# Kernel optimization log

Hardware: AMD Instinct MI355X
Metric: run time of the kernel (lower is better)

Reference implementation:

```python
import jax, jax.numpy as jnp
import numpy as np

NUM_GENO = 16384
NUM_ENV = 53
R = 2666
B = 256
EPS = 1e-5


def setup_inputs() -> dict:
    key = jax.random.key(0)
    ks = jax.random.split(key, 12)

    def w(k, shape, fan_in):
        return jax.random.normal(k, shape, dtype=jnp.float32) / np.float32(np.sqrt(fan_in))

    f32 = jnp.float32
    return {
        "x": jax.random.normal(ks[0], (B, NUM_GENO + NUM_ENV), dtype=f32),
        "W1": w(ks[1], (R, NUM_GENO), NUM_GENO), "b1": jnp.zeros((R,), f32),
        "Wmid": w(ks[2], (11, R, R), R), "bmid": jnp.zeros((11, R), f32),
        "bn_g": jnp.ones((12, R), f32), "bn_b": jnp.zeros((12, R), f32),
        "bn_rm": jnp.zeros((12, R), f32), "bn_rv": jnp.ones((12, R), f32),
        "Wlin": w(ks[3], (R, 54, NUM_ENV + 1), NUM_ENV + 1), "blin": jnp.zeros((R, 54), f32),
        "W13": w(ks[4], (54, 54), 54), "b13": jnp.zeros((54,), f32),
        "W14": w(ks[5], (54, 54), 54), "b14": jnp.zeros((54,), f32),
        "W15": w(ks[6], (5, 54), 54), "b15": jnp.zeros((5,), f32),
        "bn3_g": jnp.ones((3, R), f32), "bn3_b": jnp.zeros((3, R), f32),
        "bn3_rm": jnp.zeros((3, R), f32), "bn3_rv": jnp.ones((3, R), f32),
        "W16": w(ks[7], (750, R * 5), R * 5), "b16": jnp.zeros((750,), f32),
        "W17": w(ks[8], (750, 750), 750), "b17": jnp.zeros((750,), f32),
        "W18": w(ks[9], (750, 750), 750), "b18": jnp.zeros((750,), f32),
    }


def reference(x, W1, b1, Wmid, bmid, bn_g, bn_b, bn_rm, bn_rv, Wlin, blin,
              W13, b13, W14, b14, W15, b15, bn3_g, bn3_b, bn3_rm, bn3_rv,
              W16, b16, W17, b17, W18, b18):
    relu = jax.nn.relu

    def bn(h, i):  # BatchNorm1d eval over [B, R]
        return (h - bn_rm[i]) * jax.lax.rsqrt(bn_rv[i] + EPS) * bn_g[i] + bn_b[i]

    env = x[:, NUM_GENO:]           # [B, NUM_ENV]
    h = x[:, :NUM_GENO]             # [B, NUM_GENO]

    h = relu(bn(h @ W1.T + b1, 0))  # fc1; dropout = identity (eval)
    d = h
    k = 0
    for _block in range(5):         # residual blocks: (fc2,fc3) ... (fc10,fc11)
        for _ in range(2):
            h = relu(bn(h @ Wmid[k].T + bmid[k], k + 1))
            k += 1
        h = d + h
        d = h
    h = relu(bn(h @ Wmid[10].T + bmid[10], 11))  # fc12

    # 2666 per-feature tiny Linears fused into one batched GEMM
    # z[b,i,:] = concat(env[b], h[b,i])  -> [B, R, NUM_ENV+1]
    z = jnp.concatenate(
        [jnp.broadcast_to(env[:, None, :], (B, R, NUM_ENV)), h[:, :, None]], axis=-1)
    d3 = jnp.einsum('bif,iof->bio', z, Wlin) + blin[None]  # [B, R, 54]

    def bn3(h3, j):  # BatchNorm1d eval over [B, R, C]: channels = dim 1 (R)
        return ((h3 - bn3_rm[j][None, :, None])
                * jax.lax.rsqrt(bn3_rv[j][None, :, None] + EPS)
                * bn3_g[j][None, :, None] + bn3_b[j][None, :, None])

    h3 = relu(bn3(d3 @ W13.T + b13, 0))
    h3 = relu(bn3(h3 @ W14.T + b14, 1))
    h3 = relu(bn3(h3 @ W15.T + b15, 2))   # [B, R, 5]

    h = h3.reshape(B, -1)                  # [B, R*5]
    h = relu(h @ W16.T + b16)
    h = relu(h @ W17.T + b17)
    h = relu(h @ W18.T + b18)
    return h
```

## Files before the change

### kernel.cpp

```cpp
#include <hip/hip_runtime.h>

#define EPS 1e-5f

typedef __attribute__((ext_vector_type(8))) short s8v;
typedef __attribute__((ext_vector_type(4))) float f4v;

__device__ __forceinline__ unsigned short f2b(float x) {
  unsigned int u = __float_as_uint(x);
  u += 0x7FFFu + ((u >> 16) & 1u);
  return (unsigned short)(u >> 16);
}
__device__ __forceinline__ float b2f(unsigned short b) {
  return __uint_as_float(((unsigned int)b) << 16);
}

__global__ __launch_bounds__(256)
void gemm_bk64(const unsigned short* __restrict__ A, int lda,
               const float* __restrict__ B, int ldb,
               unsigned short* __restrict__ Pb,
               int NPAIR, int N, int K, int kchunk, int KS)
{
  __shared__ unsigned short As[256 * 72];
  __shared__ unsigned short Bs[64 * 72];
  const int bid = (int)blockIdx.x;
  const int ky = bid % KS, ntp = bid / KS;
  const int n0 = ntp << 6;
  const int t = threadIdx.x, lane = t & 63, w = t >> 6;
  const int lr = lane & 15, lk = lane >> 4;

  const int kstart = ky * kchunk;
  const int kend = min(K, kstart + kchunk);
  const int len = kend - kstart;
  const int nfull = len >> 6;
  const int rem = len & 63;

  const int ar = t >> 2, ac = t & 3;
  const int br = t >> 2, bq = t & 3;

  f4v acc[4][4] = {};
  float4 b_cur[4], b_nxt[4];

  auto loadB = [&](float4* dst, int kb) {
    const int row = n0 + br;
    if (row < N) {
      #pragma unroll
      for (int i = 0; i < 4; ++i)
        dst[i] = *(const float4*)(B + (size_t)row * ldb + kb + bq * 16 + i * 4);
    } else {
      #pragma unroll
      for (int i = 0; i < 4; ++i) { dst[i].x = dst[i].y = dst[i].z = dst[i].w = 0.f; }
    }
  };
  auto stageA = [&](int kb) {
    #pragma unroll
    for (int p = 0; p < 4; ++p) {
      const int row = ar + p * 64;
      const s8v v0 = *(const s8v*)(A + (size_t)row * lda + kb + ac * 16);
      const s8v v1 = *(const s8v*)(A + (size_t)row * lda + kb + ac * 16 + 8);
      *(s8v*)(As + row * 72 + ac * 16) = v0;
      *(s8v*)(As + row * 72 + ac * 16 + 8) = v1;
    }
  };
  auto stageB = [&](const float4* bv) {
    s8v p0, p1;
    #pragma unroll
    for (int i = 0; i < 4; ++i) {
      p0[i]     = (short)f2b(bv[i >> 1].x);
    }
    p0[0] = (short)f2b(bv[0].x); p0[1] = (short)f2b(bv[0].y);
    p0[2] = (short)f2b(bv[0].z); p0[3] = (short)f2b(bv[0].w);
    p0[4] = (short)f2b(bv[1].x); p0[5] = (short)f2b(bv[1].y);
    p0[6] = (short)f2b(bv[1].z); p0[7] = (short)f2b(bv[1].w);
    p1[0] = (short)f2b(bv[2].x); p1[1] = (short)f2b(bv[2].y);
    p1[2] = (short)f2b(bv[2].z); p1[3] = (short)f2b(bv[2].w);
    p1[4] = (short)f2b(bv[3].x); p1[5] = (short)f2b(bv[3].y);
    p1[6] = (short)f2b(bv[3].z); p1[7] = (short)f2b(bv[3].w);
    *(s8v*)(Bs + br * 72 + bq * 16) = p0;
    *(s8v*)(Bs + br * 72 + bq * 16 + 8) = p1;
  };
  auto domfma = [&]() {
    #pragma unroll
    for (int ks = 0; ks < 2; ++ks) {
      s8v af[4], bf[4];
      #pragma unroll
      for (int fm = 0; fm < 4; ++fm)
        af[fm] = *(const s8v*)(As + (w * 64 + fm * 16 + lr) * 72 + ks * 32 + lk * 8);
      #pragma unroll
      for (int fn = 0; fn < 4; ++fn)
        bf[fn] = *(const s8v*)(Bs + (fn * 16 + lr) * 72 + ks * 32 + lk * 8);
      #pragma unroll
      for (int fm = 0; fm < 4; ++fm)
        #pragma unroll
        for (int fn = 0; fn < 4; ++fn)
          acc[fm][fn] = __builtin_amdgcn_mfma_f32_16x16x32_bf16(af[fm], bf[fn], acc[fm][fn], 0, 0, 0);
    }
  };

  int kb = kstart;
  if (nfull > 0) {
    loadB(b_cur, kb);
    for (int s = 0; s < nfull; ++s) {
      stageA(kb);
      stageB(b_cur);
      __syncthreads();
      const bool more = (s + 1 < nfull);
      if (more) loadB(b_nxt, kb + 64);
      domfma();
      __syncthreads();
      if (more) {
        #pragma unroll
        for (int i = 0; i < 4; ++i) b_cur[i] = b_nxt[i];
        kb += 64;
      }
    }
    kb += 64;
  }
  if (rem) {
    stageA(kb);
    {
      const int row = n0 + br;
      #pragma unroll
      for (int i = 0; i < 4; ++i) {
        float e[4];
        #pragma unroll
        for (int v = 0; v < 4; ++v) {
          const int c = kb + bq * 16 + i * 4 + v;
          e[v] = (row < N && c < kend) ? B[(size_t)row * ldb + c] : 0.f;
        }
        b_cur[i].x = e[0]; b_cur[i].y = e[1]; b_cur[i].z = e[2]; b_cur[i].w = e[3];
      }
    }
    stageB(b_cur);
    __syncthreads();
    domfma();
    __syncthreads();
  }

  unsigned short* Pt = Pb + ((size_t)ky * NPAIR + ntp) * 16384;
  #pragma unroll
  for (int fm = 0; fm < 4; ++fm)
    #pragma unroll
    for (int fn = 0; fn < 4; ++fn) {
      const int col = fn * 16 + lr;
      #pragma unroll
      for (int j = 0; j < 4; ++j) {
        const int row = w * 64 + fm * 16 + lk * 4 + j;
        Pt[row * 64 + col] = f2b(acc[fm][fn][j]);
      }
    }
}

template<bool BN, bool RES, bool WRD, bool WRT, bool F32OUT>
__global__ __launch_bounds__(256)
void reduce_bk64(const unsigned short* __restrict__ Pb, int KS, int NPAIR, int N,
                 const float* __restrict__ bias,
                 const float* __restrict__ g, const float* __restrict__ bb,
                 const float* __restrict__ rm, const float* __restrict__ rv,
                 float* __restrict__ dR, int lddr,
                 unsigned short* __restrict__ Cb, int ldc,
                 unsigned short* __restrict__ Ct, float* __restrict__ Cf)
{
  const int bid = (int)blockIdx.x;
  const int ntp = bid >> 2, qr = bid & 3;
  const int t = threadIdx.x;
  const int row = qr * 64 + (t >> 2);
  const int c0 = (t & 3) * 16;
  const int n0 = ntp << 6;

  float vv[16];
  #pragma unroll
  for (int e = 0; e < 16; ++e) vv[e] = 0.f;

  const unsigned short* base = Pb + (size_t)ntp * 16384 + row * 64 + c0;
  for (int ky = 0; ky < KS; ++ky) {
    const s8v pa = *(const s8v*)(base + (size_t)ky * NPAIR * 16384);
    const s8v pb2 = *(const s8v*)(base + (size_t)ky * NPAIR * 16384 + 8);
    #pragma unroll
    for (int e = 0; e < 8; ++e) vv[e]     += b2f((unsigned short)pa[e]);
    #pragma unroll
    for (int e = 0; e < 8; ++e) vv[8 + e] += b2f((unsigned short)pb2[e]);
  }

  unsigned short outp[16];
  #pragma unroll
  for (int e = 0; e < 16; ++e) {
    const int col = n0 + c0 + e;
    float v = 0.f;
    if (col < N) {
      v = vv[e] + bias[col];
      if (BN) { const float s = g[col] * rsqrtf(rv[col] + EPS); v = (v - rm[col]) * s + bb[col]; }
      v = fmaxf(v, 0.f);
      if (RES) v += dR[(size_t)row * lddr + col];
      if (WRD) dR[(size_t)row * lddr + col] = v;
      if (F32OUT) Cf[(size_t)row * N + col] = v;
      else if (WRT) Ct[(size_t)col * 256 + row] = f2b(v);
    }
    outp[e] = f2b(v);
  }
  if (!F32OUT && !WRT) {
    *(s8v*)(Cb + (size_t)row * ldc + n0 + c0) = *(const s8v*)(outp);
    *(s8v*)(Cb + (size_t)row * ldc + n0 + c0 + 8) = *(const s8v*)(outp + 8);
  }
}

__global__ __launch_bounds__(256)
void prep_k(const float* __restrict__ x, unsigned short* __restrict__ xg,
            unsigned short* __restrict__ envb, unsigned short* __restrict__ h5b)
{
  const int bid = (int)blockIdx.x, t = threadIdx.x;
  if (bid < 16384) {
    const int idx = bid * 256 + t;
    const int r = idx >> 14, c = idx & 16383;
    xg[idx] = f2b(x[(size_t)r * 16437 + c]);
  } else if (bid < 16456) {
    const int idx = (bid - 16384) * 256 + t;
    const int b = idx / 72, c = idx % 72;
    envb[idx] = (c < 53) ? f2b(x[(size_t)b * 16437 + 16384 + c]) : (unsigned short)0;
  } else {
    for (int z = t; z < 256 * 46; z += 256) {
      const int b = z / 46, j = z % 46;
      h5b[(size_t)b * 13376 + 13330 + j] = 0;
    }
  }
}

__global__ __launch_bounds__(256, 2)
void fused_head(const unsigned short* __restrict__ envb,
                const unsigned short* __restrict__ htr,
                const float* __restrict__ Wlin, const float* __restrict__ blin,
                const float* __restrict__ W13, const float* __restrict__ b13,
                const float* __restrict__ W14, const float* __restrict__ b14,
                const float* __restrict__ W15, const float* __restrict__ b15,
                const float* __restrict__ bn3g, const float* __restrict__ bn3b,
                const float* __restrict__ bn3rm, const float* __restrict__ bn3rv,
                unsigned short* __restrict__ h5b)
{
  __shared__ unsigned short act[256 * 72];
  __shared__ unsigned short Wl[64 * 72];
  __shared__ unsigned short Wa[64 * 72];
  __shared__ unsigned short Wb[16 * 72];
  const int i = (int)blockIdx.x;
  const int t = threadIdx.x, lane = t & 63, w = t >> 6;
  const int lr = lane & 15, lk = lane >> 4;
  const int R = 2666;

  #pragma unroll
  for (int c8 = 0; c8 < 9; ++c8)
    *(s8v*)(act + t * 72 + c8 * 8) = *(const s8v*)(envb + t * 72 + c8 * 8);
  act[t * 72 + 53] = htr[(size_t)i * 256 + t];

  const float* wli = Wlin + (size_t)i * 2916;
  for (int idx = t; idx < 64 * 72; idx += 256) {
    const int r = idx / 72, f = idx % 72;
    Wl[idx] = (r < 54 && f < 54) ? f2b(wli[r * 54 + f]) : (unsigned short)0;
    Wa[idx] = (r < 54 && f < 54) ? f2b(W13[r * 54 + f]) : (unsigned short)0;
  }
  for (int idx = t; idx < 16 * 72; idx += 256) {
    const int r = idx / 72, f = idx % 72;
    Wb[idx] = (r < 5 && f < 54) ? f2b(W15[r * 54 + f]) : (unsigned short)0;
  }
  const float s0 = bn3g[i] * rsqrtf(bn3rv[i] + EPS), m0 = bn3rm[i], c0 = bn3b[i];
  const float s1 = bn3g[R+i] * rsqrtf(bn3rv[R+i] + EPS), m1 = bn3rm[R+i], c1 = bn3b[R+i];
  const float s2 = bn3g[2*R+i] * rsqrtf(bn3rv[2*R+i] + EPS), m2 = bn3rm[2*R+i], c2 = bn3b[2*R+i];
  __syncthreads();

  const int abase = (w * 64 + lr) * 72 + lk * 8;
  f4v acc[4][4];

  auto zacc = [&]() {
    #pragma unroll
    for (int a = 0; a < 4; ++a)
      #pragma unroll
      for (int b = 0; b < 4; ++b) acc[a][b] = f4v{0.f, 0.f, 0.f, 0.f};
  };
  auto gemm4 = [&](const unsigned short* B) {
    s8v af[2][4];
    #pragma unroll
    for (int ks = 0; ks < 2; ++ks)
      #pragma unroll
      for (int fm = 0; fm < 4; ++fm)
        af[ks][fm] = *(const s8v*)(act + abase + fm * 16 * 72 + ks * 32);
    #pragma unroll
    for (int fn = 0; fn < 4; ++fn) {
      s8v b0 = *(const s8v*)(B + (fn * 16 + lr) * 72 + lk * 8);
      s8v b1 = *(const s8v*)(B + (fn * 16 + lr) * 72 + 32 + lk * 8);
      #pragma unroll
      for (int fm = 0; fm < 4; ++fm) {
        acc[fm][fn] = __builtin_amdgcn_mfma_f32_16x16x32_bf16(af[0][fm], b0, acc[fm][fn], 0, 0, 0);
        acc[fm][fn] = __builtin_amdgcn_mfma_f32_16x16x32_bf16(af[1][fm], b1, acc[fm][fn], 0, 0, 0);
      }
    }
  };
  auto epi_bn = [&](const float* bias, float s, float m, float c) {
    #pragma unroll
    for (int fn = 0; fn < 4; ++fn) {
      const int o = fn * 16 + lr;
      const float bo = (o < 54) ? bias[o] : 0.f;
      #pragma unroll
      for (int fm = 0; fm < 4; ++fm)
        #pragma unroll
        for (int j = 0; j < 4; ++j) {
          const int row = w * 64 + fm * 16 + lk * 4 + j;
          float v = acc[fm][fn][j] + bo;
          v = (v - m) * s + c;
          v = fmaxf(v, 0.f);
          act[row * 72 + o] = (o < 54) ? f2b(v) : (unsigned short)0;
        }
    }
  };

  zacc(); gemm4(Wl);
  #pragma unroll
  for (int fn = 0; fn < 4; ++fn) {
    const int o = fn * 16 + lr;
    const float bl = (o < 54) ? blin[(size_t)i * 54 + o] : 0.f;
    #pragma unroll
    for (int fm = 0; fm < 4; ++fm)
      #pragma unroll
      for (int j = 0; j < 4; ++j) {
        const int row = w * 64 + fm * 16 + lk * 4 + j;
        float v = acc[fm][fn][j] + bl;
        act[row * 72 + o] = (o < 54) ? f2b(v) : (unsigned short)0;
      }
  }
  __syncthreads();
  for (int idx = t; idx < 64 * 72; idx += 256) {
    const int r = idx / 72, f = idx % 72;
    Wl[idx] = (r < 54 && f < 54) ? f2b(W14[r * 54 + f]) : (unsigned short)0;
  }
  zacc(); gemm4(Wa); epi_bn(b13, s0, m0, c0);
  __syncthreads();
  zacc(); gemm4(Wl); epi_bn(b14, s1, m1, c1);
  f4v a4[4] = {};
  {
    s8v af[2][4];
    #pragma unroll
    for (int ks = 0; ks < 2; ++ks)
      #pragma unroll
      for (int fm = 0; fm < 4; ++fm)
        af[ks][fm] = *(const s8v*)(act + abase + fm * 16 * 72 + ks * 32);
    s8v b0 = *(const s8v*)(Wb + lr * 72 + lk * 8);
    s8v b1 = *(const s8v*)(Wb + lr * 72 + 32 + lk * 8);
    #pragma unroll
    for (int fm = 0; fm < 4; ++fm) {
      a4[fm] = __builtin_amdgcn_mfma_f32_16x16x32_bf16(af[0][fm], b0, a4[fm], 0, 0, 0);
      a4[fm] = __builtin_amdgcn_mfma_f32_16x16x32_bf16(af[1][fm], b1, a4[fm], 0, 0, 0);
    }
  }
  if (lr < 5) {
    const float b5 = b15[lr];
    #pragma unroll
    for (int fm = 0; fm < 4; ++fm)
      #pragma unroll
      for (int j = 0; j < 4; ++j) {
        const int row = w * 64 + fm * 16 + lk * 4 + j;
        float v = a4[fm][j] + b5;
        v = (v - m2) * s2 + c2;
        v = fmaxf(v, 0.f);
        h5b[(size_t)row * 13376 + (size_t)i * 5 + lr] = f2b(v);
      }
  }
}

extern "C" void kernel_launch(void* const* d_in, const int* in_sizes, int n_in,
                              void* d_out, int out_size, void* d_ws, size_t ws_size,
                              hipStream_t stream)
{
  const float* x    = (const float*)d_in[0];
  const float* W1   = (const float*)d_in[1];
  const float* b1   = (const float*)d_in[2];
  const float* Wmid = (const float*)d_in[3];
  const float* bmid = (const float*)d_in[4];
  const float* bng  = (const float*)d_in[5];
  const float* bnb  = (const float*)d_in[6];
  const float* bnrm = (const float*)d_in[7];
  const float* bnrv = (const float*)d_in[8];
  const float* Wlin = (const float*)d_in[9];
  const float* blin = (const float*)d_in[10];
  const float* W13  = (const float*)d_in[11];
  const float* b13  = (const float*)d_in[12];
  const float* W14  = (const float*)d_in[13];
  const float* b14  = (const float*)d_in[14];
  const float* W15  = (const float*)d_in[15];
  const float* b15  = (const float*)d_in[16];
  const float* bn3g = (const float*)d_in[17];
  const float* bn3b = (const float*)d_in[18];
  const float* bn3rm= (const float*)d_in[19];
  const float* bn3rv= (const float*)d_in[20];
  const float* W16  = (const float*)d_in[21];
  const float* b16  = (const float*)d_in[22];
  const float* W17  = (const float*)d_in[23];
  const float* b17  = (const float*)d_in[24];
  const float* W18  = (const float*)d_in[25];
  const float* b18  = (const float*)d_in[26];

  const int R = 2666;
  char* p = (char*)d_ws;
  unsigned short* xg  = (unsigned short*)p; p += (size_t)256 * 16384 * 2;
  unsigned short* hA  = (unsigned short*)p; p += (size_t)256 * 2688 * 2;
  unsigned short* hB  = (unsigned short*)p; p += (size_t)256 * 2688 * 2;
  float*          dR  = (float*)p;          p += (size_t)256 * 2688 * 4;
  unsigned short* h5b = (unsigned short*)p; p += (size_t)256 * 13376 * 2;
  unsigned short* h6b = (unsigned short*)p; p += (size_t)256 * 768 * 2;
  unsigned short* h7b = (unsigned short*)p; p += (size_t)256 * 768 * 2;
  unsigned short* envb= (unsigned short*)p; p += (size_t)256 * 72 * 2;
  unsigned short* htr = (unsigned short*)p; p += (size_t)2666 * 256 * 2;
  unsigned short* Pb  = (unsigned short*)p;

  dim3 TB(256);

  prep_k<<<dim3(16457), TB, 0, stream>>>(x, xg, envb, h5b);

  gemm_bk64<<<dim3(42 * 8), TB, 0, stream>>>(xg, 16384, W1, 16384, Pb, 42, R, 16384, 2048, 8);
  reduce_bk64<true, false, true, false, false><<<dim3(42 * 4), TB, 0, stream>>>(
      Pb, 8, 42, R, b1, bng, bnb, bnrm, bnrv, dR, 2688, hA, 2688, nullptr, nullptr);

  unsigned short* cur = hA; unsigned short* nxt = hB;
  for (int k = 0; k < 11; ++k) {
    const float* bw = Wmid + (size_t)k * R * R;
    const float* bs = bmid + (size_t)k * R;
    const int L = k + 1;
    gemm_bk64<<<dim3(42 * 14), TB, 0, stream>>>(cur, 2688, bw, R, Pb, 42, R, R, 192, 14);
    if (k == 10)
      reduce_bk64<true, false, false, true, false><<<dim3(42 * 4), TB, 0, stream>>>(
          Pb, 14, 42, R, bs, bng + (size_t)L * R, bnb + (size_t)L * R,
          bnrm + (size_t)L * R, bnrv + (size_t)L * R,
          nullptr, 0, nullptr, 2688, htr, nullptr);
    else if ((k & 1) == 0)
      reduce_bk64<true, false, false, false, false><<<dim3(42 * 4), TB, 0, stream>>>(
          Pb, 14, 42, R, bs, bng + (size_t)L * R, bnb + (size_t)L * R,
          bnrm + (size_t)L * R, bnrv + (size_t)L * R,
          nullptr, 0, nxt, 2688, nullptr, nullptr);
    else
      reduce_bk64<true, true, true, false, false><<<dim3(42 * 4), TB, 0, stream>>>(
          Pb, 14, 42, R, bs, bng + (size_t)L * R, bnb + (size_t)L * R,
          bnrm + (size_t)L * R, bnrv + (size_t)L * R,
          dR, 2688, nxt, 2688, nullptr, nullptr);
    unsigned short* tmp = cur; cur = nxt; nxt = tmp;
  }

  fused_head<<<dim3(2666), TB, 0, stream>>>(
      envb, htr, Wlin, blin, W13, b13, W14, b14, W15, b15,
      bn3g, bn3b, bn3rm, bn3rv, h5b);

  gemm_bk64<<<dim3(12 * 15), TB, 0, stream>>>(h5b, 13376, W16, 13330, Pb, 12, 750, 13330, 896, 15);
  reduce_bk64<false, false, false, false, false><<<dim3(12 * 4), TB, 0, stream>>>(
      Pb, 15, 12, 750, b16, nullptr, nullptr, nullptr, nullptr,
      nullptr, 0, h6b, 768, nullptr, nullptr);

  gemm_bk64<<<dim3(12 * 6), TB, 0, stream>>>(h6b, 768, W17, 750, Pb, 12, 750, 750, 128, 6);
  reduce_bk64<false, false, false, false, false><<<dim3(12 * 4), TB, 0, stream>>>(
      Pb, 6, 12, 750, b17, nullptr, nullptr, nullptr, nullptr,
      nullptr, 0, h7b, 768, nullptr, nullptr);

  gemm_bk64<<<dim3(12 * 6), TB, 0, stream>>>(h7b, 768, W18, 750, Pb, 12, 750, 750, 128, 6);
  reduce_bk64<false, false, false, false, true><<<dim3(12 * 4), TB, 0, stream>>>(
      Pb, 6, 12, 750, b18, nullptr, nullptr, nullptr, nullptr,
      nullptr, 0, nullptr, 768, nullptr, (float*)d_out);
}
```

Baseline: 605.0 us.

## Fuse fc1 and mid-layer GEMM/reduce chain into one cooperative persistent kernel

Replaces the 24 separate split-K GEMM and reduce launches for fc1 through fc12 with a single cooperative kernel of 504 blocks. Grid-wide syncs separate each GEMM phase from its reduce phase. Split-K factors change to 12 for every layer (kchunk 1408 for fc1, 256 for the mid layers), and the host falls back to the old launch sequence if the cooperative launch fails. This removes per-launch overhead and launch gaps, at the cost of grid-sync latency, idle blocks during the reduce phases, and a requirement that all blocks be co-resident at two blocks per CU.

```diff
diff --git a/kernel.cpp b/kernel.cpp
--- a/kernel.cpp
+++ b/kernel.cpp
@@ -1,4 +1,7 @@
 #include <hip/hip_runtime.h>
+#include <hip/hip_cooperative_groups.h>
+
+namespace cg = cooperative_groups;
 
 #define EPS 1e-5f
 
@@ -12,6 +15,210 @@
 }
 __device__ __forceinline__ float b2f(unsigned short b) {
   return __uint_as_float(((unsigned int)b) << 16);
+}
+
+__global__ __launch_bounds__(256, 2)
+void coop_chain(const unsigned short* __restrict__ xg,
+                const float* __restrict__ W1, const float* __restrict__ b1,
+                const float* __restrict__ Wmid, const float* __restrict__ bmid,
+                const float* __restrict__ bng, const float* __restrict__ bnb,
+                const float* __restrict__ bnrm, const float* __restrict__ bnrv,
+                float* __restrict__ dR,
+                unsigned short* __restrict__ hA, unsigned short* __restrict__ hB,
+                unsigned short* __restrict__ htr,
+                unsigned short* __restrict__ Pb)
+{
+  cg::grid_group grid = cg::this_grid();
+  __shared__ unsigned short As[256 * 72];
+  __shared__ unsigned short Bs[64 * 72];
+  const int bid = (int)blockIdx.x;
+  const int t = threadIdx.x, lane = t & 63, w = t >> 6;
+  const int lr = lane & 15, lk = lane >> 4;
+  const int R = 2666;
+
+  const int ky = bid / 42, ntp = bid % 42;
+  const int n0 = ntp << 6;
+  const int ar = t >> 2, ac = t & 3;
+  const int br = t >> 2, bq = t & 3;
+
+  auto gemm = [&](const unsigned short* A, int lda, const float* B, int ldb,
+                  int K, int kchunk) {
+    const int kstart = ky * kchunk;
+    const int kend = min(K, kstart + kchunk);
+    const int len = kend - kstart;
+    const int nfull = (len > 0) ? (len >> 6) : 0;
+    const int rem = (len > 0) ? (len & 63) : 0;
+
+    f4v acc[4][4] = {};
+    float4 b_cur[4], b_nxt[4];
+
+    auto loadB = [&](float4* dst, int kb) {
+      const int row = n0 + br;
+      if (row < R) {
+        #pragma unroll
+        for (int i = 0; i < 4; ++i)
+          dst[i] = *(const float4*)(B + (size_t)row * ldb + kb + bq * 16 + i * 4);
+      } else {
+        #pragma unroll
+        for (int i = 0; i < 4; ++i) { dst[i].x = dst[i].y = dst[i].z = dst[i].w = 0.f; }
+      }
+    };
+    auto stageA = [&](int kb) {
+      #pragma unroll
+      for (int p = 0; p < 4; ++p) {
+        const int row = ar + p * 64;
+        const s8v v0 = *(const s8v*)(A + (size_t)row * lda + kb + ac * 16);
+        const s8v v1 = *(const s8v*)(A + (size_t)row * lda + kb + ac * 16 + 8);
+        *(s8v*)(As + row * 72 + ac * 16) = v0;
+        *(s8v*)(As + row * 72 + ac * 16 + 8) = v1;
+      }
+    };
+    auto stageB = [&](const float4* bv) {
+      s8v p0, p1;
+      p0[0] = (short)f2b(bv[0].x); p0[1] = (short)f2b(bv[0].y);
+      p0[2] = (short)f2b(bv[0].z); p0[3] = (short)f2b(bv[0].w);
+      p0[4] = (short)f2b(bv[1].x); p0[5] = (short)f2b(bv[1].y);
+      p0[6] = (short)f2b(bv[1].z); p0[7] = (short)f2b(bv[1].w);
+      p1[0] = (short)f2b(bv[2].x); p1[1] = (short)f2b(bv[2].y);
+      p1[2] = (short)f2b(bv[2].z); p1[3] = (short)f2b(bv[2].w);
+      p1[4] = (short)f2b(bv[3].x); p1[5] = (short)f2b(bv[3].y);
+      p1[6] = (short)f2b(bv[3].z); p1[7] = (short)f2b(bv[3].w);
+      *(s8v*)(Bs + br * 72 + bq * 16) = p0;
+      *(s8v*)(Bs + br * 72 + bq * 16 + 8) = p1;
+    };
+    auto domfma = [&]() {
+      #pragma unroll
+      for (int ks = 0; ks < 2; ++ks) {
+        s8v af[4], bf[4];
+        #pragma unroll
+        for (int fm = 0; fm < 4; ++fm)
+          af[fm] = *(const s8v*)(As + (w * 64 + fm * 16 + lr) * 72 + ks * 32 + lk * 8);
+        #pragma unroll
+        for (int fn = 0; fn < 4; ++fn)
+          bf[fn] = *(const s8v*)(Bs + (fn * 16 + lr) * 72 + ks * 32 + lk * 8);
+        #pragma unroll
+        for (int fm = 0; fm < 4; ++fm)
+          #pragma unroll
+          for (int fn = 0; fn < 4; ++fn)
+            acc[fm][fn] = __builtin_amdgcn_mfma_f32_16x16x32_bf16(af[fm], bf[fn], acc[fm][fn], 0, 0, 0);
+      }
+    };
+
+    int kb = kstart;
+    if (nfull > 0) {
+      loadB(b_cur, kb);
+      for (int s = 0; s < nfull; ++s) {
+        stageA(kb);
+        stageB(b_cur);
+        __syncthreads();
+        const bool more = (s + 1 < nfull);
+        if (more) loadB(b_nxt, kb + 64);
+        domfma();
+        __syncthreads();
+        if (more) {
+          #pragma unroll
+          for (int i = 0; i < 4; ++i) b_cur[i] = b_nxt[i];
+          kb += 64;
+        }
+      }
+      kb += 64;
+    }
+    if (rem) {
+      stageA(kb);
+      {
+        const int row = n0 + br;
+        #pragma unroll
+        for (int i = 0; i < 4; ++i) {
+          float e[4];
+          #pragma unroll
+          for (int v = 0; v < 4; ++v) {
+            const int c = kb + bq * 16 + i * 4 + v;
+            e[v] = (row < R && c < kend) ? B[(size_t)row * ldb + c] : 0.f;
+          }
+          b_cur[i].x = e[0]; b_cur[i].y = e[1]; b_cur[i].z = e[2]; b_cur[i].w = e[3];
+        }
+      }
+      stageB(b_cur);
+      __syncthreads();
+      domfma();
+      __syncthreads();
+    }
+
+    unsigned short* Pt = Pb + ((size_t)ky * 42 + ntp) * 16384;
+    #pragma unroll
+    for (int fm = 0; fm < 4; ++fm)
+      #pragma unroll
+      for (int fn = 0; fn < 4; ++fn) {
+        const int col = fn * 16 + lr;
+        #pragma unroll
+        for (int j = 0; j < 4; ++j) {
+          const int row = w * 64 + fm * 16 + lk * 4 + j;
+          Pt[row * 64 + col] = f2b(acc[fm][fn][j]);
+        }
+      }
+  };
+
+  auto reduce = [&](const float* bias, const float* g, const float* bb,
+                    const float* rm, const float* rv,
+                    bool RES, bool WRD, bool WRT, unsigned short* Cb) {
+    if (bid >= 168) return;
+    const int rntp = bid % 42, qr = bid / 42;
+    const int rn0 = rntp << 6;
+    const int row = qr * 64 + (t >> 2);
+    const int c0 = (t & 3) * 16;
+
+    float vv[16];
+    #pragma unroll
+    for (int e = 0; e < 16; ++e) vv[e] = 0.f;
+    const unsigned short* base = Pb + (size_t)rntp * 16384 + row * 64 + c0;
+    for (int kk = 0; kk < 12; ++kk) {
+      const s8v pa  = *(const s8v*)(base + (size_t)kk * 42 * 16384);
+      const s8v pb2 = *(const s8v*)(base + (size_t)kk * 42 * 16384 + 8);
+      #pragma unroll
+      for (int e = 0; e < 8; ++e) vv[e]     += b2f((unsigned short)pa[e]);
+      #pragma unroll
+      for (int e = 0; e < 8; ++e) vv[8 + e] += b2f((unsigned short)pb2[e]);
+    }
+    unsigned short outp[16];
+    #pragma unroll
+    for (int e = 0; e < 16; ++e) {
+      const int col = rn0 + c0 + e;
+      float v = 0.f;
+      if (col < R) {
+        v = vv[e] + bias[col];
+        const float s = g[col] * rsqrtf(rv[col] + EPS);
+        v = (v - rm[col]) * s + bb[col];
+        v = fmaxf(v, 0.f);
+        if (RES) v += dR[(size_t)row * 2688 + col];
+        if (WRD) dR[(size_t)row * 2688 + col] = v;
+        if (WRT) htr[(size_t)col * 256 + row] = f2b(v);
+      }
+      outp[e] = f2b(v);
+    }
+    if (!WRT) {
+      *(s8v*)(Cb + (size_t)row * 2688 + rn0 + c0) = *(const s8v*)(outp);
+      *(s8v*)(Cb + (size_t)row * 2688 + rn0 + c0 + 8) = *(const s8v*)(outp + 8);
+    }
+  };
+
+  gemm(xg, 16384, W1, 16384, 16384, 1408);
+  grid.sync();
+  reduce(b1, bng, bnb, bnrm, bnrv, false, true, false, hA);
+  grid.sync();
+
+  unsigned short* cur = hA;
+  unsigned short* nxt = hB;
+  for (int k = 0; k < 11; ++k) {
+    gemm(cur, 2688, Wmid + (size_t)k * R * R, R, R, 256);
+    grid.sync();
+    const int L = k + 1;
+    reduce(bmid + (size_t)k * R,
+           bng + (size_t)L * R, bnb + (size_t)L * R,
+           bnrm + (size_t)L * R, bnrv + (size_t)L * R,
+           (k & 1) != 0, (k & 1) != 0, k == 10, nxt);
+    grid.sync();
+    unsigned short* tmp = cur; cur = nxt; nxt = tmp;
+  }
 }
 
 __global__ __launch_bounds__(256)
@@ -31,8 +238,8 @@
   const int kstart = ky * kchunk;
   const int kend = min(K, kstart + kchunk);
   const int len = kend - kstart;
-  const int nfull = len >> 6;
-  const int rem = len & 63;
+  const int nfull = (len > 0) ? (len >> 6) : 0;
+  const int rem = (len > 0) ? (len & 63) : 0;
 
   const int ar = t >> 2, ac = t & 3;
   const int br = t >> 2, bq = t & 3;
@@ -63,10 +270,6 @@
   };
   auto stageB = [&](const float4* bv) {
     s8v p0, p1;
-    #pragma unroll
-    for (int i = 0; i < 4; ++i) {
-      p0[i]     = (short)f2b(bv[i >> 1].x);
-    }
     p0[0] = (short)f2b(bv[0].x); p0[1] = (short)f2b(bv[0].y);
     p0[2] = (short)f2b(bv[0].z); p0[3] = (short)f2b(bv[0].w);
     p0[4] = (short)f2b(bv[1].x); p0[5] = (short)f2b(bv[1].y);
@@ -170,17 +373,15 @@
   float vv[16];
   #pragma unroll
   for (int e = 0; e < 16; ++e) vv[e] = 0.f;
-
   const unsigned short* base = Pb + (size_t)ntp * 16384 + row * 64 + c0;
   for (int ky = 0; ky < KS; ++ky) {
-    const s8v pa = *(const s8v*)(base + (size_t)ky * NPAIR * 16384);
+    const s8v pa  = *(const s8v*)(base + (size_t)ky * NPAIR * 16384);
     const s8v pb2 = *(const s8v*)(base + (size_t)ky * NPAIR * 16384 + 8);
     #pragma unroll
     for (int e = 0; e < 8; ++e) vv[e]     += b2f((unsigned short)pa[e]);
     #pragma unroll
     for (int e = 0; e < 8; ++e) vv[8 + e] += b2f((unsigned short)pb2[e]);
   }
-
   unsigned short outp[16];
   #pragma unroll
   for (int e = 0; e < 16; ++e) {
@@ -411,32 +612,43 @@
 
   prep_k<<<dim3(16457), TB, 0, stream>>>(x, xg, envb, h5b);
 
-  gemm_bk64<<<dim3(42 * 8), TB, 0, stream>>>(xg, 16384, W1, 16384, Pb, 42, R, 16384, 2048, 8);
-  reduce_bk64<true, false, true, false, false><<<dim3(42 * 4), TB, 0, stream>>>(
-      Pb, 8, 42, R, b1, bng, bnb, bnrm, bnrv, dR, 2688, hA, 2688, nullptr, nullptr);
-
-  unsigned short* cur = hA; unsigned short* nxt = hB;
-  for (int k = 0; k < 11; ++k) {
-    const float* bw = Wmid + (size_t)k * R * R;
-    const float* bs = bmid + (size_t)k * R;
-    const int L = k + 1;
-    gemm_bk64<<<dim3(42 * 14), TB, 0, stream>>>(cur, 2688, bw, R, Pb, 42, R, R, 192, 14);
-    if (k == 10)
-      reduce_bk64<true, false, false, true, false><<<dim3(42 * 4), TB, 0, stream>>>(
-          Pb, 14, 42, R, bs, bng + (size_t)L * R, bnb + (size_t)L * R,
-          bnrm + (size_t)L * R, bnrv + (size_t)L * R,
-          nullptr, 0, nullptr, 2688, htr, nullptr);
-    else if ((k & 1) == 0)
-      reduce_bk64<true, false, false, false, false><<<dim3(42 * 4), TB, 0, stream>>>(
-          Pb, 14, 42, R, bs, bng + (size_t)L * R, bnb + (size_t)L * R,
-          bnrm + (size_t)L * R, bnrv + (size_t)L * R,
-          nullptr, 0, nxt, 2688, nullptr, nullptr);
-    else
-      reduce_bk64<true, true, true, false, false><<<dim3(42 * 4), TB, 0, stream>>>(
-          Pb, 14, 42, R, bs, bng + (size_t)L * R, bnb + (size_t)L * R,
-          bnrm + (size_t)L * R, bnrv + (size_t)L * R,
-          dR, 2688, nxt, 2688, nullptr, nullptr);
-    unsigned short* tmp = cur; cur = nxt; nxt = tmp;
+  hipError_t cerr;
+  {
+    void* args[] = {
+      (void*)&xg, (void*)&W1, (void*)&b1, (void*)&Wmid, (void*)&bmid,
+      (void*)&bng, (void*)&bnb, (void*)&bnrm, (void*)&bnrv,
+      (void*)&dR, (void*)&hA, (void*)&hB, (void*)&htr, (void*)&Pb
+    };
+    cerr = hipLaunchCooperativeKernel((const void*)coop_chain, dim3(504), TB,
+                                      args, 0, stream);
+  }
+  if (cerr != hipSuccess) {
+    gemm_bk64<<<dim3(42 * 8), TB, 0, stream>>>(xg, 16384, W1, 16384, Pb, 42, R, 16384, 2048, 8);
+    reduce_bk64<true, false, true, false, false><<<dim3(42 * 4), TB, 0, stream>>>(
+        Pb, 8, 42, R, b1, bng, bnb, bnrm, bnrv, dR, 2688, hA, 2688, nullptr, nullptr);
+    unsigned short* cur = hA; unsigned short* nxt = hB;
+    for (int k = 0; k < 11; ++k) {
+      const float* bw = Wmid + (size_t)k * R * R;
+      const float* bs = bmid + (size_t)k * R;
+      const int L = k + 1;
+      gemm_bk64<<<dim3(42 * 14), TB, 0, stream>>>(cur, 2688, bw, R, Pb, 42, R, R, 192, 14);
+      if (k == 10)
+        reduce_bk64<true, false, false, true, false><<<dim3(42 * 4), TB, 0, stream>>>(
+            Pb, 14, 42, R, bs, bng + (size_t)L * R, bnb + (size_t)L * R,
+            bnrm + (size_t)L * R, bnrv + (size_t)L * R,
+            nullptr, 0, nullptr, 2688, htr, nullptr);
+      else if ((k & 1) == 0)
+        reduce_bk64<true, false, false, false, false><<<dim3(42 * 4), TB, 0, stream>>>(
+            Pb, 14, 42, R, bs, bng + (size_t)L * R, bnb + (size_t)L * R,
+            bnrm + (size_t)L * R, bnrv + (size_t)L * R,
+            nullptr, 0, nxt, 2688, nullptr, nullptr);
+      else
+        reduce_bk64<true, true, true, false, false><<<dim3(42 * 4), TB, 0, stream>>>(
+            Pb, 14, 42, R, bs, bng + (size_t)L * R, bnb + (size_t)L * R,
+            bnrm + (size_t)L * R, bnrv + (size_t)L * R,
+            dR, 2688, nxt, 2688, nullptr, nullptr);
+      unsigned short* tmp = cur; cur = nxt; nxt = tmp;
+    }
   }
 
   fused_head<<<dim3(2666), TB, 0, stream>>>(
```

Measured after the change: 2.124 ms. 251% more time.

## Replace split-K GEMM plus reduce with direct fused-epilogue GEMM for mid layers

Applied to the files above, without the earlier changes.

Adds a gemm_direct kernel that computes a 64x64 output tile over the full K and applies bias, batchnorm, ReLU, the residual add and the output write in its epilogue. It replaces the split-K gemm plus reduce kernel pairs for the eleven 2666x2666 layers and the two 750x750 layers. This removes the bf16 partial-sum round trip through global memory and roughly halves the number of launches. In exchange the mid layers now run only 168 blocks (48 for the small layers), each with a long serial K loop, so less parallelism is available on a chip with many CUs. It also drops the bf16 rounding of partial sums.

```diff
diff --git a/kernel.cpp b/kernel.cpp
--- a/kernel.cpp
+++ b/kernel.cpp
@@ -12,6 +12,142 @@
 }
 __device__ __forceinline__ float b2f(unsigned short b) {
   return __uint_as_float(((unsigned int)b) << 16);
+}
+
+template<bool BN, bool RES, bool WRD, bool WRT, bool F32OUT>
+__global__ __launch_bounds__(256)
+void gemm_direct(const unsigned short* __restrict__ A, int lda,
+                 const float* __restrict__ B, int ldb,
+                 const float* __restrict__ bias,
+                 const float* __restrict__ g, const float* __restrict__ bb,
+                 const float* __restrict__ rm, const float* __restrict__ rv,
+                 float* __restrict__ dR, int lddr,
+                 unsigned short* __restrict__ Cb, int ldc,
+                 unsigned short* __restrict__ htr, float* __restrict__ Cf,
+                 int N, int K)
+{
+  __shared__ unsigned short As[64 * 72];
+  __shared__ unsigned short Bs[64 * 72];
+  const int bid = (int)blockIdx.x;
+  const int mr = bid & 3, nt = bid >> 2;
+  const int m0 = mr << 6, n0 = nt << 6;
+  const int t = threadIdx.x, lane = t & 63, w = t >> 6;
+  const int lr = lane & 15, lk = lane >> 4;
+  const int ar = t >> 2, ac = t & 3;
+  const int br = t >> 2, bq = t & 3;
+
+  const int nfull = K >> 6;
+  const int rem = K & 63;
+
+  f4v acc[4] = {};
+  float4 b_cur[4], b_nxt[4];
+
+  auto loadB = [&](float4* dst, int kb) {
+    const int row = n0 + br;
+    if (row < N) {
+      #pragma unroll
+      for (int i = 0; i < 4; ++i)
+        dst[i] = *(const float4*)(B + (size_t)row * ldb + kb + bq * 16 + i * 4);
+    } else {
+      #pragma unroll
+      for (int i = 0; i < 4; ++i) { dst[i].x = dst[i].y = dst[i].z = dst[i].w = 0.f; }
+    }
+  };
+  auto stageA = [&](int kb) {
+    const s8v v0 = *(const s8v*)(A + (size_t)(m0 + ar) * lda + kb + ac * 16);
+    const s8v v1 = *(const s8v*)(A + (size_t)(m0 + ar) * lda + kb + ac * 16 + 8);
+    *(s8v*)(As + ar * 72 + ac * 16) = v0;
+    *(s8v*)(As + ar * 72 + ac * 16 + 8) = v1;
+  };
+  auto stageB = [&](const float4* bv) {
+    s8v p0, p1;
+    p0[0] = (short)f2b(bv[0].x); p0[1] = (short)f2b(bv[0].y);
+    p0[2] = (short)f2b(bv[0].z); p0[3] = (short)f2b(bv[0].w);
+    p0[4] = (short)f2b(bv[1].x); p0[5] = (short)f2b(bv[1].y);
+    p0[6] = (short)f2b(bv[1].z); p0[7] = (short)f2b(bv[1].w);
+    p1[0] = (short)f2b(bv[2].x); p1[1] = (short)f2b(bv[2].y);
+    p1[2] = (short)f2b(bv[2].z); p1[3] = (short)f2b(bv[2].w);
+    p1[4] = (short)f2b(bv[3].x); p1[5] = (short)f2b(bv[3].y);
+    p1[6] = (short)f2b(bv[3].z); p1[7] = (short)f2b(bv[3].w);
+    *(s8v*)(Bs + br * 72 + bq * 16) = p0;
+    *(s8v*)(Bs + br * 72 + bq * 16 + 8) = p1;
+  };
+  auto domfma = [&]() {
+    #pragma unroll
+    for (int ks = 0; ks < 2; ++ks) {
+      s8v af = *(const s8v*)(As + (w * 16 + lr) * 72 + ks * 32 + lk * 8);
+      #pragma unroll
+      for (int fn = 0; fn < 4; ++fn) {
+        s8v bf = *(const s8v*)(Bs + (fn * 16 + lr) * 72 + ks * 32 + lk * 8);
+        acc[fn] = __builtin_amdgcn_mfma_f32_16x16x32_bf16(af, bf, acc[fn], 0, 0, 0);
+      }
+    }
+  };
+
+  int kb = 0;
+  if (nfull > 0) {
+    loadB(b_cur, 0);
+    for (int s = 0; s < nfull; ++s) {
+      stageA(kb);
+      stageB(b_cur);
+      __syncthreads();
+      const bool more = (s + 1 < nfull);
+      if (more) loadB(b_nxt, kb + 64);
+      domfma();
+      __syncthreads();
+      if (more) {
+        #pragma unroll
+        for (int i = 0; i < 4; ++i) b_cur[i] = b_nxt[i];
+        kb += 64;
+      }
+    }
+    kb += 64;
+  }
+  if (rem) {
+    stageA(kb);
+    {
+      const int row = n0 + br;
+      #pragma unroll
+      for (int i = 0; i < 4; ++i) {
+        float e[4];
+        #pragma unroll
+        for (int v = 0; v < 4; ++v) {
+          const int c = kb + bq * 16 + i * 4 + v;
+          e[v] = (row < N && c < K) ? B[(size_t)row * ldb + c] : 0.f;
+        }
+        b_cur[i].x = e[0]; b_cur[i].y = e[1]; b_cur[i].z = e[2]; b_cur[i].w = e[3];
+      }
+    }
+    stageB(b_cur);
+    __syncthreads();
+    domfma();
+    __syncthreads();
+  }
+
+  #pragma unroll
+  for (int fn = 0; fn < 4; ++fn) {
+    const int col = n0 + fn * 16 + lr;
+    const bool cin = (col < N);
+    #pragma unroll
+    for (int j = 0; j < 4; ++j) {
+      const int row = m0 + w * 16 + lk * 4 + j;
+      float v = 0.f;
+      if (cin) {
+        v = acc[fn][j] + bias[col];
+        if (BN) { const float s = g[col] * rsqrtf(rv[col] + EPS); v = (v - rm[col]) * s + bb[col]; }
+        v = fmaxf(v, 0.f);
+        if (RES) v += dR[(size_t)row * lddr + col];
+        if (WRD) dR[(size_t)row * lddr + col] = v;
+      }
+      if (WRT) {
+        if (cin) htr[(size_t)col * 256 + row] = f2b(v);
+      } else if (F32OUT) {
+        if (cin) Cf[(size_t)row * N + col] = v;
+      } else {
+        Cb[(size_t)row * ldc + col] = f2b(v);
+      }
+    }
+  }
 }
 
 __global__ __launch_bounds__(256)
@@ -31,8 +167,8 @@
   const int kstart = ky * kchunk;
   const int kend = min(K, kstart + kchunk);
   const int len = kend - kstart;
-  const int nfull = len >> 6;
-  const int rem = len & 63;
+  const int nfull = (len > 0) ? (len >> 6) : 0;
+  const int rem = (len > 0) ? (len & 63) : 0;
 
   const int ar = t >> 2, ac = t & 3;
   const int br = t >> 2, bq = t & 3;
@@ -63,10 +199,6 @@
   };
   auto stageB = [&](const float4* bv) {
     s8v p0, p1;
-    #pragma unroll
-    for (int i = 0; i < 4; ++i) {
-      p0[i]     = (short)f2b(bv[i >> 1].x);
-    }
     p0[0] = (short)f2b(bv[0].x); p0[1] = (short)f2b(bv[0].y);
     p0[2] = (short)f2b(bv[0].z); p0[3] = (short)f2b(bv[0].w);
     p0[4] = (short)f2b(bv[1].x); p0[5] = (short)f2b(bv[1].y);
@@ -150,15 +282,14 @@
     }
 }
 
-template<bool BN, bool RES, bool WRD, bool WRT, bool F32OUT>
+template<bool BN, bool WRD>
 __global__ __launch_bounds__(256)
 void reduce_bk64(const unsigned short* __restrict__ Pb, int KS, int NPAIR, int N,
                  const float* __restrict__ bias,
                  const float* __restrict__ g, const float* __restrict__ bb,
                  const float* __restrict__ rm, const float* __restrict__ rv,
                  float* __restrict__ dR, int lddr,
-                 unsigned short* __restrict__ Cb, int ldc,
-                 unsigned short* __restrict__ Ct, float* __restrict__ Cf)
+                 unsigned short* __restrict__ Cb, int ldc)
 {
   const int bid = (int)blockIdx.x;
   const int ntp = bid >> 2, qr = bid & 3;
@@ -170,17 +301,15 @@
   float vv[16];
   #pragma unroll
   for (int e = 0; e < 16; ++e) vv[e] = 0.f;
-
   const unsigned short* base = Pb + (size_t)ntp * 16384 + row * 64 + c0;
   for (int ky = 0; ky < KS; ++ky) {
-    const s8v pa = *(const s8v*)(base + (size_t)ky * NPAIR * 16384);
+    const s8v pa  = *(const s8v*)(base + (size_t)ky * NPAIR * 16384);
     const s8v pb2 = *(const s8v*)(base + (size_t)ky * NPAIR * 16384 + 8);
     #pragma unroll
     for (int e = 0; e < 8; ++e) vv[e]     += b2f((unsigned short)pa[e]);
     #pragma unroll
     for (int e = 0; e < 8; ++e) vv[8 + e] += b2f((unsigned short)pb2[e]);
   }
-
   unsigned short outp[16];
   #pragma unroll
   for (int e = 0; e < 16; ++e) {
@@ -190,17 +319,12 @@
       v = vv[e] + bias[col];
       if (BN) { const float s = g[col] * rsqrtf(rv[col] + EPS); v = (v - rm[col]) * s + bb[col]; }
       v = fmaxf(v, 0.f);
-      if (RES) v += dR[(size_t)row * lddr + col];
       if (WRD) dR[(size_t)row * lddr + col] = v;
-      if (F32OUT) Cf[(size_t)row * N + col] = v;
-      else if (WRT) Ct[(size_t)col * 256 + row] = f2b(v);
     }
     outp[e] = f2b(v);
   }
-  if (!F32OUT && !WRT) {
-    *(s8v*)(Cb + (size_t)row * ldc + n0 + c0) = *(const s8v*)(outp);
-    *(s8v*)(Cb + (size_t)row * ldc + n0 + c0 + 8) = *(const s8v*)(outp + 8);
-  }
+  *(s8v*)(Cb + (size_t)row * ldc + n0 + c0) = *(const s8v*)(outp);
+  *(s8v*)(Cb + (size_t)row * ldc + n0 + c0 + 8) = *(const s8v*)(outp + 8);
 }
 
 __global__ __launch_bounds__(256)
@@ -412,30 +536,29 @@
   prep_k<<<dim3(16457), TB, 0, stream>>>(x, xg, envb, h5b);
 
   gemm_bk64<<<dim3(42 * 8), TB, 0, stream>>>(xg, 16384, W1, 16384, Pb, 42, R, 16384, 2048, 8);
-  reduce_bk64<true, false, true, false, false><<<dim3(42 * 4), TB, 0, stream>>>(
-      Pb, 8, 42, R, b1, bng, bnb, bnrm, bnrv, dR, 2688, hA, 2688, nullptr, nullptr);
+  reduce_bk64<true, true><<<dim3(42 * 4), TB, 0, stream>>>(
+      Pb, 8, 42, R, b1, bng, bnb, bnrm, bnrv, dR, 2688, hA, 2688);
 
   unsigned short* cur = hA; unsigned short* nxt = hB;
   for (int k = 0; k < 11; ++k) {
     const float* bw = Wmid + (size_t)k * R * R;
     const float* bs = bmid + (size_t)k * R;
     const int L = k + 1;
-    gemm_bk64<<<dim3(42 * 14), TB, 0, stream>>>(cur, 2688, bw, R, Pb, 42, R, R, 192, 14);
     if (k == 10)
-      reduce_bk64<true, false, false, true, false><<<dim3(42 * 4), TB, 0, stream>>>(
-          Pb, 14, 42, R, bs, bng + (size_t)L * R, bnb + (size_t)L * R,
+      gemm_direct<true, false, false, true, false><<<dim3(4 * 42), TB, 0, stream>>>(
+          cur, 2688, bw, R, bs, bng + (size_t)L * R, bnb + (size_t)L * R,
           bnrm + (size_t)L * R, bnrv + (size_t)L * R,
-          nullptr, 0, nullptr, 2688, htr, nullptr);
+          dR, 2688, nxt, 2688, htr, nullptr, R, R);
     else if ((k & 1) == 0)
-      reduce_bk64<true, false, false, false, false><<<dim3(42 * 4), TB, 0, stream>>>(
-          Pb, 14, 42, R, bs, bng + (size_t)L * R, bnb + (size_t)L * R,
+      gemm_direct<true, false, false, false, false><<<dim3(4 * 42), TB, 0, stream>>>(
+          cur, 2688, bw, R, bs, bng + (size_t)L * R, bnb + (size_t)L * R,
           bnrm + (size_t)L * R, bnrv + (size_t)L * R,
-          nullptr, 0, nxt, 2688, nullptr, nullptr);
+          dR, 2688, nxt, 2688, nullptr, nullptr, R, R);
     else
-      reduce_bk64<true, true, true, false, false><<<dim3(42 * 4), TB, 0, stream>>>(
-          Pb, 14, 42, R, bs, bng + (size_t)L * R, bnb + (size_t)L * R,
+      gemm_direct<true, true, true, false, false><<<dim3(4 * 42), TB, 0, stream>>>(
+          cur, 2688, bw, R, bs, bng + (size_t)L * R, bnb + (size_t)L * R,
           bnrm + (size_t)L * R, bnrv + (size_t)L * R,
-          dR, 2688, nxt, 2688, nullptr, nullptr);
+          dR, 2688, nxt, 2688, nullptr, nullptr, R, R);
     unsigned short* tmp = cur; cur = nxt; nxt = tmp;
   }
 
@@ -444,17 +567,14 @@
       bn3g, bn3b, bn3rm, bn3rv, h5b);
 
   gemm_bk64<<<dim3(12 * 15), TB, 0, stream>>>(h5b, 13376, W16, 13330, Pb, 12, 750, 13330, 896, 15);
-  reduce_bk64<false, false, false, false, false><<<dim3(12 * 4), TB, 0, stream>>>(
-      Pb, 15, 12, 750, b16, nullptr, nullptr, nullptr, nullptr,
-      nullptr, 0, h6b, 768, nullptr, nullptr);
-
-  gemm_bk64<<<dim3(12 * 6), TB, 0, stream>>>(h6b, 768, W17, 750, Pb, 12, 750, 750, 128, 6);
-  reduce_bk64<false, false, false, false, false><<<dim3(12 * 4), TB, 0, stream>>>(
-      Pb, 6, 12, 750, b17, nullptr, nullptr, nullptr, nullptr,
-      nullptr, 0, h7b, 768, nullptr, nullptr);
-
-  gemm_bk64<<<dim3(12 * 6), TB, 0, stream>>>(h7b, 768, W18, 750, Pb, 12, 750, 750, 128, 6);
-  reduce_bk64<false, false, false, false, true><<<dim3(12 * 4), TB, 0, stream>>>(
-      Pb, 6, 12, 750, b18, nullptr, nullptr, nullptr, nullptr,
-      nullptr, 0, nullptr, 768, nullptr, (float*)d_out);
-}
+  reduce_bk64<false, false><<<dim3(12 * 4), TB, 0, stream>>>(
+      Pb, 15, 12, 750, b16, nullptr, nullptr, nullptr, nullptr, nullptr, 0, h6b, 768);
+
+  gemm_direct<false, false, false, false, false><<<dim3(4 * 12), TB, 0, stream>>>(
+      h6b, 768, W17, 750, b17, nullptr, nullptr, nullptr, nullptr,
+      nullptr, 0, h7b, 768, nullptr, nullptr, 750, 750);
+
+  gemm_direct<false, false, false, false, true><<<dim3(4 * 12), TB, 0, stream>>>(
+      h7b, 768, W18, 750, b18, nullptr, nullptr, nullptr, nullptr,
+      nullptr, 0, nullptr, 768, nullptr, (float*)d_out, 750, 750);
+}
```

Measured after the change: 818.6 us. +35.3%, slower.
